# Kernel tuning notes

Hardware: AMD Instinct MI355X
Metric: run time of the kernel (lower is better)

The kernel has to match this reference:

```python
import jax, jax.numpy as jnp
import numpy as np

N_NODES = 100000
N_EDGES = 1600000
IN_DIM = 128
OUT_DIM = 64
HEADS = 4
NEG_SLOPE = 0.2  # PyG GATConv default
LN_EPS = 1e-5


def setup_inputs() -> dict:
    key = jax.random.key(0)
    ks = jax.random.split(key, 8)
    x = jax.random.normal(ks[0], (N_NODES, IN_DIM), dtype=jnp.float32)
    edge_index = jax.random.randint(ks[1], (2, N_EDGES), 0, N_NODES, dtype=jnp.int64)
    # GATConv params: lin weight, per-head attention vectors, output bias (concat=False)
    s = 1.0 / np.sqrt(IN_DIM)
    W = jax.random.uniform(ks[2], (IN_DIM, HEADS * OUT_DIM), jnp.float32, -s, s)
    att_src = jax.random.uniform(ks[3], (HEADS, OUT_DIM), jnp.float32, -s, s)
    att_dst = jax.random.uniform(ks[4], (HEADS, OUT_DIM), jnp.float32, -s, s)
    bias = jnp.zeros((OUT_DIM,), jnp.float32)
    gamma = jnp.ones((OUT_DIM,), jnp.float32)
    beta = jnp.zeros((OUT_DIM,), jnp.float32)
    return {"x": x, "edge_index": edge_index, "W": W, "att_src": att_src,
            "att_dst": att_dst, "bias": bias, "gamma": gamma, "beta": beta}


def reference(x, edge_index, W, att_src, att_dst, bias, gamma, beta):
    N = x.shape[0]
    H, C = att_src.shape
    # Linear projection, split heads: (N, H, C)
    xl = (x @ W).reshape(N, H, C)
    # Per-node attention logits: (N, H)
    a_src = jnp.einsum('nhc,hc->nh', xl, att_src)
    a_dst = jnp.einsum('nhc,hc->nh', xl, att_dst)
    # Add self-loops (PyG GATConv default add_self_loops=True)
    loops = jnp.arange(N, dtype=edge_index.dtype)
    src = jnp.concatenate([edge_index[0], loops])  # (E+N,)
    dst = jnp.concatenate([edge_index[1], loops])
    # Per-edge attention: gather, leaky_relu, segment softmax over destination
    alpha = jax.nn.leaky_relu(a_src[src] + a_dst[dst], NEG_SLOPE)  # (E+N, H)
    amax = jax.ops.segment_max(alpha, dst, num_segments=N)  # (N, H)
    e = jnp.exp(alpha - amax[dst])
    denom = jax.ops.segment_sum(e, dst, num_segments=N)  # (N, H)
    alpha = e / (denom[dst] + 1e-16)
    # Message passing: scatter-add alpha-weighted source features to dst
    msg = xl[src] * alpha[:, :, None]  # (E+N, H, C)
    out = jax.ops.segment_sum(msg, dst, num_segments=N)  # (N, H, C)
    out = out.mean(axis=1) + bias  # concat=False -> head average, (N, C)
    # LayerNorm
    mu = out.mean(axis=-1, keepdims=True)
    var = out.var(axis=-1, keepdims=True)
    return (out - mu) * jax.lax.rsqrt(var + LN_EPS) * gamma + beta
```

## Files before the change

kernel.cpp:

```cpp
#include <hip/hip_runtime.h>
#include <hip/hip_fp16.h>

#define IN_DIM   128
#define HC       256
#define OUT_DIM  64
#define HEADS    4
#define NEG_SLOPE 0.2f
#define LN_EPS   1e-5f
#define DBITS    6
#define DPB      64
#define MAXBINS  2048
#define CAP      2048
#define NHIST    256
#define SCAT_TPE 16

typedef short bf16x8 __attribute__((ext_vector_type(8)));
typedef float f32x4  __attribute__((ext_vector_type(4)));

__device__ __forceinline__ float lrelu(float a){ return a > 0.f ? a : NEG_SLOPE * a; }

__device__ __forceinline__ unsigned short f2bf(float f){
  unsigned u = __float_as_uint(f);
  u = u + 0x7fffu + ((u >> 16) & 1u);
  return (unsigned short)(u >> 16);
}
__device__ __forceinline__ unsigned pk2(float a, float b){
  return (unsigned)f2bf(a) | ((unsigned)f2bf(b) << 16);
}
__device__ __forceinline__ __half2 u2h(unsigned u){ return *(__half2*)&u; }
__device__ __forceinline__ unsigned h2u(__half2 h){ return *(unsigned*)&h; }

__device__ __forceinline__ bool detect32(const int* ei){
  int ln = threadIdx.x & 63;
  unsigned probe = (ln < 32) ? (unsigned)ei[2*ln + 1] : 0u;
  return __ballot(probe != 0) != 0ull;
}

__global__ __launch_bounds__(256) void k_front(
    const float* __restrict__ W, unsigned short* __restrict__ Wt,
    const int* ei, int* __restrict__ bincnt, int E, int nbins)
{
  if (blockIdx.x < 128){
    int n = blockIdx.x*2 + (threadIdx.x >> 7);
    int k = threadIdx.x & 127;
    Wt[n*IN_DIM + k] = f2bf(W[k*HC + n]);
    return;
  }
  __shared__ int h[MAXBINS];
  bool i32 = detect32(ei);
  for (int i = threadIdx.x; i < nbins; i += 256) h[i] = 0;
  __syncthreads();
  int slot = blockIdx.x - 128;
  if (i32){
    const int* dstp = ei + E;
    for (int e = slot*256 + threadIdx.x; e < E; e += NHIST*256)
      atomicAdd(&h[dstp[e] >> DBITS], 1);
  } else {
    const long long* dstp = (const long long*)ei + E;
    for (int e = slot*256 + threadIdx.x; e < E; e += NHIST*256)
      atomicAdd(&h[((int)dstp[e]) >> DBITS], 1);
  }
  __syncthreads();
  for (int i = threadIdx.x; i < nbins; i += 256)
    if (h[i]) atomicAdd(&bincnt[i], h[i]);
}

__global__ __launch_bounds__(1024) void k_binscan(const int* __restrict__ bincnt,
    int* binstart, int* bincur, int nbins, int E)
{
  __shared__ int sh[1024];
  int t = threadIdx.x;
  int i0 = 2*t, i1 = 2*t + 1;
  int a = (i0 < nbins) ? bincnt[i0] : 0;
  int b = (i1 < nbins) ? bincnt[i1] : 0;
  int s = a + b;
  sh[t] = s; __syncthreads();
  #pragma unroll
  for (int off = 1; off < 1024; off <<= 1){
    int v = (t >= off) ? sh[t-off] : 0;
    __syncthreads();
    sh[t] += v;
    __syncthreads();
  }
  int ex = sh[t] - s;
  if (i0 < nbins){ binstart[i0] = ex;     bincur[i0] = ex; }
  if (i1 < nbins){ binstart[i1] = ex + a; bincur[i1] = ex + a; }
  if (t == 0) binstart[nbins] = E;
}

__device__ __forceinline__ void gemm_body(int bid, char* smem,
    const float* __restrict__ x, const unsigned short* __restrict__ Wt,
    const float* __restrict__ att_s, const float* __restrict__ att_d,
    __half* __restrict__ xl_t, float* __restrict__ a_src,
    float* __restrict__ a_dst, int N)
{
  unsigned short* sxl = (unsigned short*)(smem + 16384);
  int t = threadIdx.x;
  int nb = bid * 64;

  #pragma unroll
  for (int it = 0; it < 4; ++it){
    int idx = it*256 + t;
    int row = idx >> 4, seg = idx & 15;
    uint4 pk = make_uint4(0,0,0,0);
    if (nb + row < N){
      const float* xr = x + (size_t)(nb + row)*IN_DIM + seg*8;
      float4 f0 = *(const float4*)xr;
      float4 f1 = *(const float4*)(xr + 4);
      pk.x = pk2(f0.x, f0.y); pk.y = pk2(f0.z, f0.w);
      pk.z = pk2(f1.x, f1.y); pk.w = pk2(f1.z, f1.w);
    }
    int byte = (row*256 + seg*16) ^ ((row & 7) << 4);
    *(uint4*)(smem + byte) = pk;
  }
  __syncthreads();

  int w = t >> 6, l = t & 63;

  bf16x8 bfr[4][4];
  #pragma unroll
  for (int nt = 0; nt < 4; ++nt){
    int col = w*64 + nt*16 + (l & 15);
    #pragma unroll
    for (int ks = 0; ks < 4; ++ks)
      bfr[nt][ks] = *(const bf16x8*)(Wt + (size_t)col*IN_DIM + ks*32 + ((l >> 4) << 3));
  }
  float attS[4], attD[4];
  #pragma unroll
  for (int nt = 0; nt < 4; ++nt){
    attS[nt] = att_s[w*64 + nt*16 + (l & 15)];
    attD[nt] = att_d[w*64 + nt*16 + (l & 15)];
  }

  #pragma unroll
  for (int sub = 0; sub < 4; ++sub){
    bf16x8 afr[4];
    #pragma unroll
    for (int ks = 0; ks < 4; ++ks){
      int row = sub*16 + (l & 15);
      int byte = (row*256 + ks*64 + ((l >> 4) << 4)) ^ ((row & 7) << 4);
      afr[ks] = *(const bf16x8*)(smem + byte);
    }
    f32x4 acc[4] = {{0,0,0,0},{0,0,0,0},{0,0,0,0},{0,0,0,0}};
    #pragma unroll
    for (int nt = 0; nt < 4; ++nt)
      #pragma unroll
      for (int ks = 0; ks < 4; ++ks)
        acc[nt] = __builtin_amdgcn_mfma_f32_16x16x32_bf16(afr[ks], bfr[nt][ks], acc[nt], 0, 0, 0);

    #pragma unroll
    for (int r = 0; r < 4; ++r){
      float ps = 0.f, pd = 0.f;
      #pragma unroll
      for (int nt = 0; nt < 4; ++nt){
        ps = fmaf(acc[nt][r], attS[nt], ps);
        pd = fmaf(acc[nt][r], attD[nt], pd);
      }
      #pragma unroll
      for (int o = 8; o; o >>= 1){ ps += __shfl_xor(ps, o); pd += __shfl_xor(pd, o); }
      int node = nb + sub*16 + (l >> 4)*4 + r;
      if ((l & 15) == 0 && node < N){
        a_src[node*4 + w] = ps;
        a_dst[node*4 + w] = pd;
      }
    }

    #pragma unroll
    for (int nt = 0; nt < 4; ++nt){
      int ch = nt*16 + (l & 15);
      #pragma unroll
      for (int r = 0; r < 4; ++r){
        int row = (l >> 4)*4 + r;
        sxl[row*HC + ch*4 + w] = __half_as_ushort(__float2half(acc[nt][r]));
      }
    }
    __syncthreads();
    const uint4* s4 = (const uint4*)sxl;
    uint4* g4 = (uint4*)(xl_t + (size_t)(nb + sub*16)*HC);
    #pragma unroll
    for (int c = t; c < 512; c += 256){
      int row = c >> 5;
      if (nb + sub*16 + row < N) g4[c] = s4[c];
    }
    __syncthreads();
  }
}

__device__ __forceinline__ void scat_body(int bid, char* smem,
    const int* ei, int* bincur, unsigned* tmp, int E, int nbins)
{
  int* h    = (int*)smem;
  int* base = (int*)(smem + MAXBINS*4);
  bool i32 = detect32(ei);
  int tile0 = bid * (256*SCAT_TPE);
  for (int i = threadIdx.x; i < nbins; i += 256) h[i] = 0;
  __syncthreads();
  unsigned pk[SCAT_TPE]; int rk[SCAT_TPE];
  #pragma unroll
  for (int k = 0; k < SCAT_TPE; ++k){
    int e = tile0 + k*256 + threadIdx.x;
    if (e < E){
      int s, d;
      if (i32){ s = ei[e]; d = ei[E + e]; }
      else {
        s = (int)((const long long*)ei)[e];
        d = (int)((const long long*)ei)[(size_t)E + e];
      }
      int b = d >> DBITS;
      pk[k] = (unsigned)s | ((unsigned)(d & (DPB-1)) << 20);
      rk[k] = atomicAdd(&h[b], 1) | (b << 16);
    }
  }
  __syncthreads();
  for (int i = threadIdx.x; i < nbins; i += 256)
    base[i] = h[i] ? atomicAdd(&bincur[i], h[i]) : 0;
  __syncthreads();
  #pragma unroll
  for (int k = 0; k < SCAT_TPE; ++k){
    int e = tile0 + k*256 + threadIdx.x;
    if (e < E){
      int b = rk[k] >> 16, r = rk[k] & 0xFFFF;
      tmp[base[b] + r] = pk[k];
    }
  }
}

__global__ __launch_bounds__(256) void k_gemm_scat(
    const float* __restrict__ x, const unsigned short* __restrict__ Wt,
    const float* __restrict__ att_s, const float* __restrict__ att_d,
    __half* __restrict__ xl_t, float* __restrict__ a_src, float* __restrict__ a_dst,
    int N, const int* ei, int* bincur, unsigned* tmp, int E, int nbins,
    int gemmBlocks)
{
  __shared__ char smem[24576];
  int bid = (int)blockIdx.x;
  if (bid < gemmBlocks)
    gemm_body(bid, smem, x, Wt, att_s, att_d, xl_t, a_src, a_dst, N);
  else
    scat_body(bid - gemmBlocks, smem, ei, bincur, tmp, E, nbins);
}

__global__ __launch_bounds__(256) void k_node(
    const int* __restrict__ binstart, const unsigned* __restrict__ tmp,
    int* __restrict__ csr,
    const float4* __restrict__ a_src4, const float4* __restrict__ a_dst4,
    const __half* __restrict__ xl_t,
    const float* __restrict__ bias, const float* __restrict__ gamma,
    const float* __restrict__ beta, float* __restrict__ out, int N)
{
  __shared__ int cnt[DPB], sc[DPB], cur[DPB];
  __shared__ int lcsr[CAP];
  __shared__ uint2 wlds[16][16];
  int b = blockIdx.x, tid = threadIdx.x;
  int s0 = binstart[b], s1 = binstart[b+1];
  int seg = s1 - s0;

  if (tid < DPB) cnt[tid] = 0;
  __syncthreads();
  for (int e = s0 + tid; e < s1; e += 256)
    atomicAdd(&cnt[(tmp[e] >> 20) & (DPB-1)], 1);
  __syncthreads();
  if (tid < DPB) sc[tid] = cnt[tid];
  __syncthreads();
  #pragma unroll
  for (int off = 1; off < DPB; off <<= 1){
    int v = (tid < DPB && tid >= off) ? sc[tid-off] : 0;
    __syncthreads();
    if (tid < DPB) sc[tid] += v;
    __syncthreads();
  }
  if (tid < DPB){ int ex = sc[tid] - cnt[tid]; sc[tid] = ex; cur[tid] = ex; }
  __syncthreads();

  int* ebuf = (seg <= CAP) ? lcsr : (csr + s0);
  for (int e = s0 + tid; e < s1; e += 256){
    unsigned u = tmp[e];
    int dl = (u >> 20) & (DPB-1);
    int r = atomicAdd(&cur[dl], 1);
    ebuf[r] = (int)(u & 0xFFFFFu);
  }
  __syncthreads();

  int gg = tid >> 4, i = tid & 15;
  for (int n = 0; n < 4; ++n){
    int dl = gg*4 + n;
    int node = b*DPB + dl;
    if (node >= N) continue;
    int lstart = sc[dl], lend = lstart + cnt[dl];

    float4 ad  = a_dst4[node];
    float4 asl = a_src4[node];
    float es0 = __expf(lrelu(asl.x + ad.x));
    float es1 = __expf(lrelu(asl.y + ad.y));
    float es2 = __expf(lrelu(asl.z + ad.z));
    float es3 = __expf(lrelu(asl.w + ad.w));

    __half2 s01 = __floats2half2_rn(es0, es1);
    __half2 s23 = __floats2half2_rn(es2, es3);
    const uint4* ps = (const uint4*)((const char*)xl_t + ((size_t)node*512 + (i << 5)));
    uint4 xa = ps[0], xb = ps[1];
    __half2 acc[8];
    acc[0] = __hmul2(s01, u2h(xa.x));
    acc[1] = __hmul2(s23, u2h(xa.y));
    acc[2] = __hmul2(s01, u2h(xa.z));
    acc[3] = __hmul2(s23, u2h(xa.w));
    acc[4] = __hmul2(s01, u2h(xb.x));
    acc[5] = __hmul2(s23, u2h(xb.y));
    acc[6] = __hmul2(s01, u2h(xb.z));
    acc[7] = __hmul2(s23, u2h(xb.w));
    float lp0 = 0.f, lp1 = 0.f, lp2 = 0.f, lp3 = 0.f;

    for (int t2 = lstart; t2 < lend; t2 += 16){
      int rem = lend - t2; if (rem > 16) rem = 16;
      float e0 = 0.f, e1 = 0.f, e2 = 0.f, e3 = 0.f;
      if (i < rem){
        int sid = ebuf[t2 + i];
        float4 as4 = a_src4[sid];
        e0 = __expf(lrelu(as4.x + ad.x));
        e1 = __expf(lrelu(as4.y + ad.y));
        e2 = __expf(lrelu(as4.z + ad.z));
        e3 = __expf(lrelu(as4.w + ad.w));
        lp0 += e0; lp1 += e1; lp2 += e2; lp3 += e3;
      }
      wlds[gg][i] = make_uint2(h2u(__floats2half2_rn(e0, e1)),
                               h2u(__floats2half2_rn(e2, e3)));

      #pragma unroll 2
      for (int j = 0; j < rem; ++j){
        uint2 wpk = wlds[gg][j];
        int sj = ebuf[t2 + j];
        __half2 w01 = u2h(wpk.x), w23 = u2h(wpk.y);
        const uint4* p = (const uint4*)((const char*)xl_t + ((size_t)sj*512 + (i << 5)));
        uint4 ya = p[0], yb = p[1];
        acc[0] = __hfma2(w01, u2h(ya.x), acc[0]);
        acc[1] = __hfma2(w23, u2h(ya.y), acc[1]);
        acc[2] = __hfma2(w01, u2h(ya.z), acc[2]);
        acc[3] = __hfma2(w23, u2h(ya.w), acc[3]);
        acc[4] = __hfma2(w01, u2h(yb.x), acc[4]);
        acc[5] = __hfma2(w23, u2h(yb.y), acc[5]);
        acc[6] = __hfma2(w01, u2h(yb.z), acc[6]);
        acc[7] = __hfma2(w23, u2h(yb.w), acc[7]);
      }
    }

    __half2 lp01 = __floats2half2_rn(lp0, lp1);
    __half2 lp23 = __floats2half2_rn(lp2, lp3);
    #pragma unroll
    for (int o = 8; o; o >>= 1){
      lp01 = __hadd2(lp01, u2h(__shfl_xor(h2u(lp01), o)));
      lp23 = __hadd2(lp23, u2h(__shfl_xor(h2u(lp23), o)));
    }
    float r0 = __builtin_amdgcn_rcpf(__low2float(lp01) + es0);
    float r1 = __builtin_amdgcn_rcpf(__high2float(lp01) + es1);
    float r2 = __builtin_amdgcn_rcpf(__low2float(lp23) + es2);
    float r3 = __builtin_amdgcn_rcpf(__high2float(lp23) + es3);

    float4 b4 = *(const float4*)(bias + 4*i);
    float o0 = 0.25f*(__low2float(acc[0])*r0 + __high2float(acc[0])*r1 +
                      __low2float(acc[1])*r2 + __high2float(acc[1])*r3) + b4.x;
    float o1 = 0.25f*(__low2float(acc[2])*r0 + __high2float(acc[2])*r1 +
                      __low2float(acc[3])*r2 + __high2float(acc[3])*r3) + b4.y;
    float o2 = 0.25f*(__low2float(acc[4])*r0 + __high2float(acc[4])*r1 +
                      __low2float(acc[5])*r2 + __high2float(acc[5])*r3) + b4.z;
    float o3 = 0.25f*(__low2float(acc[6])*r0 + __high2float(acc[6])*r1 +
                      __low2float(acc[7])*r2 + __high2float(acc[7])*r3) + b4.w;

    float s  = o0 + o1 + o2 + o3;
    float sq = o0*o0 + o1*o1 + o2*o2 + o3*o3;
    #pragma unroll
    for (int o = 8; o; o >>= 1){
      s  += __shfl_xor(s, o);
      sq += __shfl_xor(sq, o);
    }
    float mu = s * (1.f/OUT_DIM);
    float var = sq * (1.f/OUT_DIM) - mu*mu;
    float rs = rsqrtf(var + LN_EPS);
    float4 g4v = *(const float4*)(gamma + 4*i);
    float4 be4 = *(const float4*)(beta + 4*i);
    float4 ov;
    ov.x = (o0 - mu)*rs*g4v.x + be4.x;
    ov.y = (o1 - mu)*rs*g4v.y + be4.y;
    ov.z = (o2 - mu)*rs*g4v.z + be4.z;
    ov.w = (o3 - mu)*rs*g4v.w + be4.w;
    *(float4*)(out + (size_t)node*OUT_DIM + 4*i) = ov;
  }
}

extern "C" void kernel_launch(void* const* d_in, const int* in_sizes, int n_in,
                              void* d_out, int out_size, void* d_ws, size_t ws_size,
                              hipStream_t stream)
{
  const float* x     = (const float*)d_in[0];
  const int*   ei    = (const int*)d_in[1];
  const float* W     = (const float*)d_in[2];
  const float* att_s = (const float*)d_in[3];
  const float* att_d = (const float*)d_in[4];
  const float* bias  = (const float*)d_in[5];
  const float* gamma = (const float*)d_in[6];
  const float* beta  = (const float*)d_in[7];
  float* out = (float*)d_out;

  int N = in_sizes[0] / IN_DIM;
  int E = in_sizes[1] / 2;
  int nbins = (N + DPB - 1) >> DBITS;

  char* ws = (char*)d_ws;
  __half* xl_t = (__half*)ws;                   ws += (size_t)N*HC*sizeof(__half);
  float* a_src = (float*)ws;                    ws += (size_t)N*HEADS*sizeof(float);
  float* a_dst = (float*)ws;                    ws += (size_t)N*HEADS*sizeof(float);
  int* csr      = (int*)ws;                     ws += (size_t)E*sizeof(int);
  unsigned* tmp = (unsigned*)ws;                ws += (size_t)E*sizeof(unsigned);
  int* bincnt   = (int*)ws;                     ws += MAXBINS*sizeof(int);
  int* binstart = (int*)ws;                     ws += (MAXBINS+1)*sizeof(int);
  int* bincur   = (int*)ws;                     ws += MAXBINS*sizeof(int);
  unsigned short* Wt = (unsigned short*)ws;     ws += (size_t)HC*IN_DIM*sizeof(unsigned short);

  int gemmBlocks = (N + 63)/64;
  int scatBlocks = (E + 256*SCAT_TPE - 1)/(256*SCAT_TPE);

  hipMemsetAsync(bincnt, 0, (size_t)nbins*sizeof(int), stream);
  k_front   <<<128 + NHIST, 256, 0, stream>>>(W, Wt, ei, bincnt, E, nbins);
  k_binscan <<<1, 1024, 0, stream>>>(bincnt, binstart, bincur, nbins, E);
  k_gemm_scat<<<gemmBlocks + scatBlocks, 256, 0, stream>>>(
      x, Wt, att_s, att_d, xl_t, a_src, a_dst, N, ei, bincur, tmp, E, nbins,
      gemmBlocks);
  k_node    <<<nbins, 256, 0, stream>>>(binstart, tmp, csr,
              (const float4*)a_src, (const float4*)a_dst, xl_t,
              bias, gamma, beta, out, N);
}
```

Before: 221.3 us.

## Halve destination bin size and pack scatter histogram counters into 16-bit

```diff
diff --git a/kernel.cpp b/kernel.cpp
--- a/kernel.cpp
+++ b/kernel.cpp
@@ -7,10 +7,10 @@
 #define HEADS    4
 #define NEG_SLOPE 0.2f
 #define LN_EPS   1e-5f
-#define DBITS    6
-#define DPB      64
-#define MAXBINS  2048
-#define CAP      2048
+#define DBITS    5
+#define DPB      32
+#define MAXBINS  4096
+#define CAP      768
 #define NHIST    256
 #define SCAT_TPE 16
 
@@ -70,21 +70,28 @@
 {
   __shared__ int sh[1024];
   int t = threadIdx.x;
-  int i0 = 2*t, i1 = 2*t + 1;
-  int a = (i0 < nbins) ? bincnt[i0] : 0;
-  int b = (i1 < nbins) ? bincnt[i1] : 0;
-  int s = a + b;
+  int v[4]; int s = 0;
+  #pragma unroll
+  for (int k = 0; k < 4; ++k){
+    int i = 4*t + k;
+    v[k] = (i < nbins) ? bincnt[i] : 0;
+    s += v[k];
+  }
   sh[t] = s; __syncthreads();
   #pragma unroll
   for (int off = 1; off < 1024; off <<= 1){
-    int v = (t >= off) ? sh[t-off] : 0;
-    __syncthreads();
-    sh[t] += v;
-    __syncthreads();
-  }
-  int ex = sh[t] - s;
-  if (i0 < nbins){ binstart[i0] = ex;     bincur[i0] = ex; }
-  if (i1 < nbins){ binstart[i1] = ex + a; bincur[i1] = ex + a; }
+    int u = (t >= off) ? sh[t-off] : 0;
+    __syncthreads();
+    sh[t] += u;
+    __syncthreads();
+  }
+  int run = sh[t] - s;
+  #pragma unroll
+  for (int k = 0; k < 4; ++k){
+    int i = 4*t + k;
+    if (i < nbins){ binstart[i] = run; bincur[i] = run; }
+    run += v[k];
+  }
   if (t == 0) binstart[nbins] = E;
 }
 
@@ -189,11 +196,11 @@
 __device__ __forceinline__ void scat_body(int bid, char* smem,
     const int* ei, int* bincur, unsigned* tmp, int E, int nbins)
 {
-  int* h    = (int*)smem;
-  int* base = (int*)(smem + MAXBINS*4);
+  int* h32  = (int*)smem;
+  int* base = (int*)(smem + 8192);
   bool i32 = detect32(ei);
   int tile0 = bid * (256*SCAT_TPE);
-  for (int i = threadIdx.x; i < nbins; i += 256) h[i] = 0;
+  for (int i = threadIdx.x; i < ((nbins+1)>>1); i += 256) h32[i] = 0;
   __syncthreads();
   unsigned pk[SCAT_TPE]; int rk[SCAT_TPE];
   #pragma unroll
@@ -208,18 +215,22 @@
       }
       int b = d >> DBITS;
       pk[k] = (unsigned)s | ((unsigned)(d & (DPB-1)) << 20);
-      rk[k] = atomicAdd(&h[b], 1) | (b << 16);
-    }
-  }
-  __syncthreads();
-  for (int i = threadIdx.x; i < nbins; i += 256)
-    base[i] = h[i] ? atomicAdd(&bincur[i], h[i]) : 0;
+      int sh = (b & 1) << 4;
+      unsigned old = (unsigned)atomicAdd(&h32[b >> 1], 1 << sh);
+      rk[k] = (int)((old >> sh) & 0xFFFFu) | (b << 12);
+    }
+  }
+  __syncthreads();
+  for (int i = threadIdx.x; i < nbins; i += 256){
+    int c = (h32[i >> 1] >> ((i & 1) << 4)) & 0xFFFF;
+    base[i] = c ? atomicAdd(&bincur[i], c) : 0;
+  }
   __syncthreads();
   #pragma unroll
   for (int k = 0; k < SCAT_TPE; ++k){
     int e = tile0 + k*256 + threadIdx.x;
     if (e < E){
-      int b = rk[k] >> 16, r = rk[k] & 0xFFFF;
+      int b = rk[k] >> 12, r = rk[k] & 0xFFF;
       tmp[base[b] + r] = pk[k];
     }
   }
@@ -255,7 +266,7 @@
   int s0 = binstart[b], s1 = binstart[b+1];
   int seg = s1 - s0;
 
-  if (tid < DPB) cnt[tid] = 0;
+  if (tid < DPB){ cnt[tid] = 0; }
   __syncthreads();
   for (int e = s0 + tid; e < s1; e += 256)
     atomicAdd(&cnt[(tmp[e] >> 20) & (DPB-1)], 1);
@@ -282,8 +293,9 @@
   __syncthreads();
 
   int gg = tid >> 4, i = tid & 15;
-  for (int n = 0; n < 4; ++n){
-    int dl = gg*4 + n;
+  #pragma unroll
+  for (int n = 0; n < 2; ++n){
+    int dl = gg*2 + n;
     int node = b*DPB + dl;
     if (node >= N) continue;
     int lstart = sc[dl], lend = lstart + cnt[dl];
@@ -325,7 +337,7 @@
       wlds[gg][i] = make_uint2(h2u(__floats2half2_rn(e0, e1)),
                                h2u(__floats2half2_rn(e2, e3)));
 
-      #pragma unroll 2
+      #pragma unroll 4
       for (int j = 0; j < rem; ++j){
         uint2 wpk = wlds[gg][j];
         int sj = ebuf[t2 + j];
```

New measurement: 219.2 us, median of 2. Within noise of the previous version (-1.0%).
